# Kernel tuning notes

Measured on AMD Instinct MI355X. Metric: run time of the kernel, lower is better.

The kernel has to match this reference:

```python
import jax, jax.numpy as jnp
import numpy as np

L = 2000          # number of residues (sequence length)
FEATURES_L = 2048 # config.features_L pad target
W = 7             # config.window_size
D = 54            # per-residue feature dim after bert_lin
H = 3             # attention heads
HD = D // H       # head dim = 18
CH = 32           # conv hidden channels
KS = (3, 5, 7)    # config.kernels


def setup_inputs() -> dict:
    key = jax.random.key(0)
    ks = jax.random.split(key, 20)
    n = lambda k, s, sc=0.02: jax.random.normal(k, s, jnp.float32) * sc
    return {
        'beft_f': jax.random.normal(ks[0], (L, 1024), jnp.float32),
        'pssm_f': jax.random.normal(ks[1], (L, 20), jnp.float32),
        'hmm_f': jax.random.normal(ks[2], (L, 30), jnp.float32),
        'dssp_f': jax.random.normal(ks[3], (L, 14), jnp.float32),
        'W_bert': n(ks[4], (1024, D)), 'b_bert': jnp.zeros((D,), jnp.float32),
        'ln_g1': jnp.ones((D,), jnp.float32), 'ln_b1': jnp.zeros((D,), jnp.float32),
        'ln_g2': jnp.ones((D,), jnp.float32), 'ln_b2': jnp.zeros((D,), jnp.float32),
        'conv1_w': n(ks[5], (CH, 1, 3, 1), 0.1), 'conv1_b': n(ks[6], (CH,), 0.1),
        'prelu_a': jnp.array(0.25, jnp.float32),
        'conv2_w': n(ks[7], (CH, 1, 5, 1), 0.1), 'conv2_b': n(ks[8], (CH,), 0.1),
        'conv3_w': n(ks[9], (CH, 1, 7, 1), 0.1), 'conv3_b': n(ks[10], (CH,), 0.1),
        'W1': n(ks[11], (972, 256)), 'b1': jnp.zeros((256,), jnp.float32),
        'W2': n(ks[12], (CH * 256, 256)), 'b2': jnp.zeros((256,), jnp.float32),
    }


def _ln(x, g, b, eps=1e-5):
    m = x.mean(-1, keepdims=True)
    v = ((x - m) ** 2).mean(-1, keepdims=True)
    return (x - m) * jax.lax.rsqrt(v + eps) * g + b


def _attn(x, g, b):
    # x: (L, W, D); no qkv projections, no 1/sqrt(d) scaling (as in source)
    qh = x.reshape(x.shape[0], W, H, HD)
    s = jnp.einsum('bqhd,bkhd->bhqk', qh, qh)
    p = jax.nn.softmax(s, axis=-1)
    o = jnp.einsum('bhqk,bkhd->bqhd', p, qh).reshape(x.shape[0], W, D)
    return _ln(o, g, b)


def _conv_branch(x, w, bias, k, act):
    pad = (k - 1) // 2
    c = jax.lax.conv_general_dilated(x, w, (1, 1), ((pad, pad), (0, 0)),
                                     dimension_numbers=('NCHW', 'OIHW', 'NCHW'))
    c = act(c + bias[None, :, None, None])
    c = jax.lax.reduce_window(c, -jnp.inf, jax.lax.max,
                              (1, 1, k, 1), (1, 1, 1, 1), 'VALID')
    return c.reshape(c.shape[0], CH, -1)  # (FEATURES_L, 32, (W-k+1)*2D)


def _forward(beft_f, W_bert, b_bert, ln_g1, ln_b1, ln_g2, ln_b2,
             conv1_w, conv1_b, prelu_a, conv2_w, conv2_b, conv3_w, conv3_b,
             W1, b1, W2, b2):
    f = beft_f @ W_bert + b_bert  # (L, 54)
    # sliding-window gather replicating the source python loop exactly:
    # interior rows i in (W, L-W): window = f[i-4 : i+3]; boundary rows: [f[i], 0...0]
    i = jnp.arange(L)
    j = jnp.arange(W)
    gidx = jnp.clip(i[:, None] - (W // 2 + 1) + j[None, :], 0, L - 1)
    win_int = f[gidx]                                   # (L, 7, 54)
    win_bnd = jnp.zeros((L, W, D), f.dtype).at[:, 0].set(f)
    boundary = (i <= W) | (i + W >= L)
    new_f = jnp.where(boundary[:, None, None], win_bnd, win_int)
    sf = _attn(new_f, ln_g1, ln_b1)
    sf = _attn(sf, ln_g2, ln_b2)
    cat = jnp.concatenate([new_f, sf], axis=2)          # (L, 7, 108)
    x = jnp.pad(cat, ((0, FEATURES_L - L), (0, 0), (0, 0)))[:, None]  # (FL,1,7,108)
    prelu = lambda z: jnp.where(z >= 0, z, prelu_a * z)
    feats = jnp.concatenate([
        _conv_branch(x, conv1_w, conv1_b, KS[0], prelu),
        _conv_branch(x, conv2_w, conv2_b, KS[1], jax.nn.relu),
        _conv_branch(x, conv3_w, conv3_b, KS[2], jax.nn.relu)], axis=2)  # (FL,32,972)
    y = feats[:L] @ W1 + b1                             # (L, 32, 256)
    y = y.reshape(L, CH * 256) @ W2 + b2                # (L, 256)
    return jnp.where(y >= 0, y, 0.01 * y)               # leaky_relu


def reference(beft_f, pssm_f, hmm_f, dssp_f, W_bert, b_bert, ln_g1, ln_b1,
              ln_g2, ln_b2, conv1_w, conv1_b, prelu_a, conv2_w, conv2_b,
              conv3_w, conv3_b, W1, b1, W2, b2):
    # pssm_f / hmm_f / dssp_f are accepted but unused in the source forward
    return _forward(beft_f, W_bert, b_bert, ln_g1, ln_b1, ln_g2, ln_b2,
                    conv1_w, conv1_b, prelu_a, conv2_w, conv2_b,
                    conv3_w, conv3_b, W1, b1, W2, b2)
```

## Files before the change

### kernel.cpp

```cpp
#include <hip/hip_runtime.h>

#define L_RES 2000
#define DF 54
#define WIN 7

typedef short bf16x8 __attribute__((ext_vector_type(8)));
typedef float f32x4 __attribute__((ext_vector_type(4)));
typedef unsigned short ushort8v __attribute__((ext_vector_type(8)));

__device__ __forceinline__ unsigned short f2bf(float f) {
    unsigned int u = __float_as_uint(f);
    unsigned int r = (u + 0x7FFFu + ((u >> 16) & 1u)) >> 16;
    return (unsigned short)r;
}
__device__ __forceinline__ float bf2f(unsigned short h) {
    return __uint_as_float(((unsigned int)h) << 16);
}

__global__ __launch_bounds__(256) void split_beft(const float* __restrict__ beft,
                                                  unsigned short* __restrict__ A2) {
    int l = blockIdx.x;
    int t = threadIdx.x;
    unsigned short* row = A2 + (size_t)l * 3072;
    for (int k = t; k < 1024; k += 256) {
        unsigned short hi = 0, lo = 0;
        if (l < L_RES) {
            float x = beft[(size_t)l * 1024 + k];
            hi = f2bf(x);
            lo = f2bf(x - bf2f(hi));
        }
        row[k] = hi;
        row[1024 + k] = lo;
        row[2048 + k] = hi;
    }
}

__global__ __launch_bounds__(256) void b2t_build(const float* __restrict__ Wb,
                                                 unsigned short* __restrict__ B2T) {
    int idx = blockIdx.x * 256 + threadIdx.x;
    int n = idx / 3072, col = idx % 3072;
    int seg = col >> 10, k = col & 1023;
    unsigned short r = 0;
    if (n < DF) {
        float v = Wb[(size_t)k * DF + n];
        unsigned short hi = f2bf(v);
        r = (seg < 2) ? hi : f2bf(v - bf2f(hi));
    }
    B2T[idx] = r;
}

__global__ __launch_bounds__(256) void bert_mfma(const unsigned short* __restrict__ A2,
                                                 const unsigned short* __restrict__ B2T,
                                                 const float* __restrict__ bb,
                                                 float* __restrict__ f) {
    __shared__ unsigned short ldsA[128 * 64];
    __shared__ unsigned short ldsB[64 * 64];
    int t = threadIdx.x, w = t >> 6, lane = t & 63;
    int m0 = blockIdx.x * 128;
    int wr = w >> 1, wc = w & 1;
    int arow = lane & 15, kgrp = lane >> 4;

    const unsigned short* aS[4]; const unsigned short* bS[2];
    int aD[4], bD[2];
    #pragma unroll
    for (int j = 0; j < 4; ++j) {
        int s = j * 256 + t, r = s >> 3, c = s & 7;
        aS[j] = A2 + (size_t)(m0 + r) * 3072 + c * 8;
        aD[j] = r * 64 + ((c ^ (r & 7)) * 8);
    }
    #pragma unroll
    for (int j = 0; j < 2; ++j) {
        int s = j * 256 + t, r = s >> 3, c = s & 7;
        bS[j] = B2T + (size_t)r * 3072 + c * 8;
        bD[j] = r * 64 + ((c ^ (r & 7)) * 8);
    }
    f32x4 acc[4][2];
    #pragma unroll
    for (int mi = 0; mi < 4; ++mi)
        #pragma unroll
        for (int ni = 0; ni < 2; ++ni) acc[mi][ni] = (f32x4)(0.f);

    ushort8v va[4], vb[2];
    #pragma unroll
    for (int j = 0; j < 4; ++j) va[j] = *(const ushort8v*)(aS[j]);
    #pragma unroll
    for (int j = 0; j < 2; ++j) vb[j] = *(const ushort8v*)(bS[j]);

    for (int ks = 0; ks < 48; ++ks) {
        __syncthreads();
        #pragma unroll
        for (int j = 0; j < 4; ++j) *(ushort8v*)&ldsA[aD[j]] = va[j];
        #pragma unroll
        for (int j = 0; j < 2; ++j) *(ushort8v*)&ldsB[bD[j]] = vb[j];
        __syncthreads();
        if (ks + 1 < 48) {
            #pragma unroll
            for (int j = 0; j < 4; ++j) va[j] = *(const ushort8v*)(aS[j] + (ks + 1) * 64);
            #pragma unroll
            for (int j = 0; j < 2; ++j) vb[j] = *(const ushort8v*)(bS[j] + (ks + 1) * 64);
        }
        #pragma unroll
        for (int kk = 0; kk < 2; ++kk) {
            int chunk = kk * 4 + kgrp;
            bf16x8 af[4], bfr[2];
            #pragma unroll
            for (int mi = 0; mi < 4; ++mi) {
                int rl = wr * 64 + mi * 16 + arow;
                af[mi] = *(const bf16x8*)&ldsA[rl * 64 + ((chunk ^ (rl & 7)) * 8)];
            }
            #pragma unroll
            for (int ni = 0; ni < 2; ++ni) {
                int rl = wc * 32 + ni * 16 + arow;
                bfr[ni] = *(const bf16x8*)&ldsB[rl * 64 + ((chunk ^ (rl & 7)) * 8)];
            }
            #pragma unroll
            for (int mi = 0; mi < 4; ++mi)
                #pragma unroll
                for (int ni = 0; ni < 2; ++ni)
                    acc[mi][ni] = __builtin_amdgcn_mfma_f32_16x16x32_bf16(af[mi], bfr[ni], acc[mi][ni], 0, 0, 0);
        }
    }
    #pragma unroll
    for (int ni = 0; ni < 2; ++ni) {
        int n = wc * 32 + ni * 16 + arow;
        if (n < DF) {
            float bv = bb[n];
            #pragma unroll
            for (int mi = 0; mi < 4; ++mi)
                #pragma unroll
                for (int r = 0; r < 4; ++r) {
                    int m = m0 + wr * 64 + mi * 16 + kgrp * 4 + r;
                    if (m < L_RES) f[(size_t)m * DF + n] = acc[mi][ni][r] + bv;
                }
        }
    }
}

__device__ __forceinline__ void attn_layer_w(const float (*in)[DF], float (*out)[DF],
                                             float (*s)[WIN][WIN],
                                             const float* __restrict__ g,
                                             const float* __restrict__ b,
                                             float* mm, float* vv, int lane) {
    for (int idx = lane; idx < 3 * WIN * WIN; idx += 64) {
        int h = idx / 49, r = idx % 49, q = r / WIN, k = r % WIN;
        float sum = 0.f;
        #pragma unroll
        for (int d = 0; d < 18; ++d) sum = fmaf(in[q][h * 18 + d], in[k][h * 18 + d], sum);
        s[h][q][k] = sum;
    }
    __syncthreads();
    for (int idx = lane; idx < 3 * WIN; idx += 64) {
        int h = idx / WIN, q = idx % WIN;
        float mx = s[h][q][0];
        #pragma unroll
        for (int k = 1; k < WIN; ++k) mx = fmaxf(mx, s[h][q][k]);
        float e[WIN], sum = 0.f;
        #pragma unroll
        for (int k = 0; k < WIN; ++k) { e[k] = expf(s[h][q][k] - mx); sum += e[k]; }
        float inv = 1.f / sum;
        #pragma unroll
        for (int k = 0; k < WIN; ++k) s[h][q][k] = e[k] * inv;
    }
    __syncthreads();
    for (int idx = lane; idx < WIN * DF; idx += 64) {
        int q = idx / DF, c = idx % DF, h = c / 18;
        float sum = 0.f;
        #pragma unroll
        for (int k = 0; k < WIN; ++k) sum = fmaf(s[h][q][k], in[k][c], sum);
        out[q][c] = sum;
    }
    __syncthreads();
    for (int q = lane; q < WIN; q += 64) {
        float m = 0.f;
        for (int c = 0; c < DF; ++c) m += out[q][c];
        m *= (1.f / DF);
        float v = 0.f;
        for (int c = 0; c < DF; ++c) { float d0 = out[q][c] - m; v = fmaf(d0, d0, v); }
        v *= (1.f / DF);
        mm[q] = m; vv[q] = rsqrtf(v + 1e-5f);
    }
    __syncthreads();
    for (int idx = lane; idx < WIN * DF; idx += 64) {
        int q = idx / DF, c = idx % DF;
        out[q][c] = (out[q][c] - mm[q]) * vv[q] * g[c] + b[c];
    }
    __syncthreads();
}

__global__ __launch_bounds__(256) void window_attn4(const float* __restrict__ f,
                                                    const float* __restrict__ g1,
                                                    const float* __restrict__ b1,
                                                    const float* __restrict__ g2,
                                                    const float* __restrict__ b2,
                                                    float* __restrict__ cat) {
    int wv = threadIdx.x >> 6, lane = threadIdx.x & 63;
    int l = blockIdx.x * 4 + wv;
    __shared__ float w[4][WIN][DF], o1[4][WIN][DF], o2[4][WIN][DF];
    __shared__ float s[4][3][WIN][WIN];
    __shared__ float mm[4][WIN], vvv[4][WIN];
    bool boundary = (l <= WIN) || (l + WIN >= L_RES);
    for (int idx = lane; idx < WIN * DF; idx += 64) {
        int j = idx / DF, d = idx % DF;
        w[wv][j][d] = boundary ? (j == 0 ? f[(size_t)l * DF + d] : 0.f)
                               : f[(size_t)(l - 4 + j) * DF + d];
    }
    __syncthreads();
    attn_layer_w(w[wv], o1[wv], s[wv], g1, b1, mm[wv], vvv[wv], lane);
    attn_layer_w(o1[wv], o2[wv], s[wv], g2, b2, mm[wv], vvv[wv], lane);
    for (int idx = lane; idx < WIN * DF; idx += 64) {
        int j = idx / DF, d = idx % DF;
        cat[(size_t)l * 756 + j * 108 + d] = w[wv][j][d];
        cat[(size_t)l * 756 + j * 108 + DF + d] = o2[wv][j][d];
    }
}

__global__ __launch_bounds__(256) void transpose_to_bf16(const float* __restrict__ src,
                                                         unsigned short* __restrict__ dst,
                                                         int M, int N, int Mpad) {
    __shared__ float tile[32][33];
    int m0 = blockIdx.x * 32, n0 = blockIdx.y * 32;
    int c = threadIdx.x % 32, r0 = threadIdx.x / 32;
    #pragma unroll
    for (int rr = 0; rr < 4; ++rr) {
        int r = r0 + rr * 8, m = m0 + r;
        tile[r][c] = (m < M) ? src[(size_t)m * N + n0 + c] : 0.f;
    }
    __syncthreads();
    #pragma unroll
    for (int rr = 0; rr < 4; ++rr) {
        int r = r0 + rr * 8;
        dst[(size_t)(n0 + r) * Mpad + m0 + c] = f2bf(tile[c][r]);
    }
}

__global__ __launch_bounds__(256) void zero_pad_rows(unsigned int* __restrict__ p) {
    int i = blockIdx.x * 256 + threadIdx.x;
    if (i < 196608) p[i] = 0u;
}

__global__ __launch_bounds__(256) void conv_pool(
        const float* __restrict__ cat,
        const float* __restrict__ c1w, const float* __restrict__ c1b,
        const float* __restrict__ pa_p,
        const float* __restrict__ c2w, const float* __restrict__ c2b,
        const float* __restrict__ c3w, const float* __restrict__ c3b,
        unsigned short* __restrict__ Ap, int lbase) {
    int l = lbase + blockIdx.x;
    int t = threadIdx.x;
    __shared__ float catl[756];
    for (int i = t; i < 756; i += 256) catl[i] = cat[(size_t)l * 756 + i];
    __syncthreads();
    float pa = pa_p[0];
    size_t rowbase = (size_t)blockIdx.x * 32;
    for (int idx = t; idx < 3456; idx += 256) {
        int c = idx / 108, d = idx - c * 108;
        unsigned short* Arow = Ap + (rowbase + c) * 1024;
        float col[WIN];
        #pragma unroll
        for (int h = 0; h < WIN; ++h) col[h] = catl[h * 108 + d];
        {
            float w0 = c1w[c * 3], w1 = c1w[c * 3 + 1], w2 = c1w[c * 3 + 2], bb = c1b[c];
            float v[WIN];
            #pragma unroll
            for (int h = 0; h < WIN; ++h) {
                float sum = bb;
                if (h >= 1) sum = fmaf(w0, col[h - 1], sum);
                sum = fmaf(w1, col[h], sum);
                if (h <= 5) sum = fmaf(w2, col[h + 1], sum);
                v[h] = sum >= 0.f ? sum : pa * sum;
            }
            #pragma unroll
            for (int p = 0; p < 5; ++p)
                Arow[p * 108 + d] = f2bf(fmaxf(fmaxf(v[p], v[p + 1]), v[p + 2]));
        }
        {
            float wg[5], bb = c2b[c];
            #pragma unroll
            for (int x = 0; x < 5; ++x) wg[x] = c2w[c * 5 + x];
            float v[WIN];
            #pragma unroll
            for (int h = 0; h < WIN; ++h) {
                float sum = bb;
                #pragma unroll
                for (int x = 0; x < 5; ++x) {
                    int hh = h + x - 2;
                    if (hh >= 0 && hh <= 6) sum = fmaf(wg[x], col[hh], sum);
                }
                v[h] = fmaxf(sum, 0.f);
            }
            #pragma unroll
            for (int p = 0; p < 3; ++p) {
                float mx = v[p];
                #pragma unroll
                for (int r = 1; r < 5; ++r) mx = fmaxf(mx, v[p + r]);
                Arow[540 + p * 108 + d] = f2bf(mx);
            }
        }
        {
            float wg[7], bb = c3b[c];
            #pragma unroll
            for (int x = 0; x < 7; ++x) wg[x] = c3w[c * 7 + x];
            float mx = 0.f;
            #pragma unroll
            for (int h = 0; h < WIN; ++h) {
                float sum = bb;
                #pragma unroll
                for (int x = 0; x < 7; ++x) {
                    int hh = h + x - 3;
                    if (hh >= 0 && hh <= 6) sum = fmaf(wg[x], col[hh], sum);
                }
                mx = fmaxf(mx, fmaxf(sum, 0.f));
            }
            Arow[864 + d] = f2bf(mx);
        }
    }
    for (int i = t; i < 832; i += 256) {
        int r = i / 26, q = i - r * 26;
        *(unsigned int*)&Ap[(rowbase + r) * 1024 + 972 + q * 2] = 0u;
    }
}

template<bool EPI_BF16, int ZBITS>
__global__ __launch_bounds__(512) void gemm_tile8(
        const unsigned short* __restrict__ A, long lda,
        const unsigned short* __restrict__ B, long ldb,
        int nk, const float* __restrict__ bias,
        unsigned short* __restrict__ outB, float* __restrict__ outF,
        long outRowBase) {
    __shared__ unsigned short ldsA[128 * 64];
    __shared__ unsigned short ldsB[256 * 64];
    int t = threadIdx.x, w = t >> 6, lane = t & 63;
    int bid = blockIdx.x;
    int z = bid & ((1 << ZBITS) - 1);
    long m0 = (long)(bid >> ZBITS) * 128;
    long koff = (long)z * (long)nk * 64;
    A += koff; B += koff;
    int wr = w >> 2, wc = w & 3;
    int arow = lane & 15, kgrp = lane >> 4;

    const unsigned short* aS[2]; const unsigned short* bS[4];
    int aD[2], bD[4];
    #pragma unroll
    for (int j = 0; j < 2; ++j) {
        int s = j * 512 + t, r = s >> 3, c = s & 7;
        aS[j] = A + (size_t)(m0 + r) * lda + c * 8;
        aD[j] = r * 64 + ((c ^ (r & 7)) * 8);
    }
    #pragma unroll
    for (int j = 0; j < 4; ++j) {
        int s = j * 512 + t, r = s >> 3, c = s & 7;
        bS[j] = B + (size_t)r * ldb + c * 8;
        bD[j] = r * 64 + ((c ^ (r & 7)) * 8);
    }
    f32x4 acc[4][4];
    #pragma unroll
    for (int mi = 0; mi < 4; ++mi)
        #pragma unroll
        for (int ni = 0; ni < 4; ++ni) acc[mi][ni] = (f32x4)(0.f);

    ushort8v va[2], vb[4];
    #pragma unroll
    for (int j = 0; j < 2; ++j) va[j] = *(const ushort8v*)(aS[j]);
    #pragma unroll
    for (int j = 0; j < 4; ++j) vb[j] = *(const ushort8v*)(bS[j]);

    for (int ks = 0; ks < nk; ++ks) {
        __syncthreads();
        #pragma unroll
        for (int j = 0; j < 2; ++j) *(ushort8v*)&ldsA[aD[j]] = va[j];
        #pragma unroll
        for (int j = 0; j < 4; ++j) *(ushort8v*)&ldsB[bD[j]] = vb[j];
        __syncthreads();
        if (ks + 1 < nk) {
            #pragma unroll
            for (int j = 0; j < 2; ++j) va[j] = *(const ushort8v*)(aS[j] + (ks + 1) * 64);
            #pragma unroll
            for (int j = 0; j < 4; ++j) vb[j] = *(const ushort8v*)(bS[j] + (ks + 1) * 64);
        }
        #pragma unroll
        for (int kk = 0; kk < 2; ++kk) {
            int chunk = kk * 4 + kgrp;
            bf16x8 af[4], bfr[4];
            #pragma unroll
            for (int mi = 0; mi < 4; ++mi) {
                int rl = wr * 64 + mi * 16 + arow;
                af[mi] = *(const bf16x8*)&ldsA[rl * 64 + ((chunk ^ (rl & 7)) * 8)];
            }
            #pragma unroll
            for (int ni = 0; ni < 4; ++ni) {
                int rl = wc * 64 + ni * 16 + arow;
                bfr[ni] = *(const bf16x8*)&ldsB[rl * 64 + ((chunk ^ (rl & 7)) * 8)];
            }
            #pragma unroll
            for (int mi = 0; mi < 4; ++mi)
                #pragma unroll
                for (int ni = 0; ni < 4; ++ni)
                    acc[mi][ni] = __builtin_amdgcn_mfma_f32_16x16x32_bf16(af[mi], bfr[ni], acc[mi][ni], 0, 0, 0);
        }
    }
    #pragma unroll
    for (int ni = 0; ni < 4; ++ni) {
        int n = wc * 64 + ni * 16 + arow;
        float bv = EPI_BF16 ? bias[n] : 0.f;
        #pragma unroll
        for (int mi = 0; mi < 4; ++mi)
            #pragma unroll
            for (int r = 0; r < 4; ++r) {
                long m = m0 + wr * 64 + mi * 16 + kgrp * 4 + r;
                if (EPI_BF16)
                    outB[(outRowBase + m) * 256 + n] = f2bf(acc[mi][ni][r] + bv);
                else
                    outF[((long)z * 2048 + m) * 256 + n] = acc[mi][ni][r];
            }
    }
}

__global__ __launch_bounds__(256) void reduce2(const float* __restrict__ part,
                                               const float* __restrict__ b2v,
                                               float* __restrict__ out) {
    int l = blockIdx.x, n = threadIdx.x;
    float sum = b2v[n];
    #pragma unroll
    for (int s = 0; s < 8; ++s) sum += part[((size_t)s * 2048 + l) * 256 + n];
    out[(size_t)l * 256 + n] = sum >= 0.f ? sum : 0.01f * sum;
}

extern "C" void kernel_launch(void* const* d_in, const int* in_sizes, int n_in,
                              void* d_out, int out_size, void* d_ws, size_t ws_size,
                              hipStream_t stream) {
    const float* beft = (const float*)d_in[0];
    const float* Wb  = (const float*)d_in[4];
    const float* bb  = (const float*)d_in[5];
    const float* g1  = (const float*)d_in[6];
    const float* b1  = (const float*)d_in[7];
    const float* g2  = (const float*)d_in[8];
    const float* b2  = (const float*)d_in[9];
    const float* c1w = (const float*)d_in[10];
    const float* c1b = (const float*)d_in[11];
    const float* pa  = (const float*)d_in[12];
    const float* c2w = (const float*)d_in[13];
    const float* c2b = (const float*)d_in[14];
    const float* c3w = (const float*)d_in[15];
    const float* c3b = (const float*)d_in[16];
    const float* W1  = (const float*)d_in[17];
    const float* b1v = (const float*)d_in[18];
    const float* W2  = (const float*)d_in[19];
    const float* b2v = (const float*)d_in[20];
    float* out = (float*)d_out;
    char* ws = (char*)d_ws;

    float*          f    = (float*)(ws + 0);
    float*          cat  = (float*)(ws + 524288);
    unsigned short* W1T  = (unsigned short*)(ws + 8388608);
    unsigned short* W2T  = (unsigned short*)(ws + 8912896);
    unsigned short* y1   = (unsigned short*)(ws + 13107200);
    unsigned short* A2   = (unsigned short*)(ws + 13107200);
    unsigned short* B2T  = (unsigned short*)(ws + 25690112);
    unsigned short* Ap   = (unsigned short*)(ws + 46661632);
    float*          part = (float*)(ws + 46661632);

    long avail = (long)ws_size - 46661632L;
    long tpc = avail / (128L * 1024L * 2L);
    if (tpc < 1) tpc = 1;
    if (tpc > 500) tpc = 500;

    split_beft<<<2048, 256, 0, stream>>>(beft, A2);
    b2t_build<<<768, 256, 0, stream>>>(Wb, B2T);
    bert_mfma<<<16, 256, 0, stream>>>(A2, B2T, bb, f);
    window_attn4<<<500, 256, 0, stream>>>(f, g1, b1, g2, b2, cat);
    transpose_to_bf16<<<dim3(32, 8), 256, 0, stream>>>(W1, W1T, 972, 256, 1024);
    transpose_to_bf16<<<dim3(256, 8), 256, 0, stream>>>(W2, W2T, 8192, 256, 8192);
    zero_pad_rows<<<768, 256, 0, stream>>>((unsigned int*)(y1 + (size_t)2000 * 8192));

    for (long t0 = 0; t0 < 500; t0 += tpc) {
        long nt = (500 - t0 < tpc) ? (500 - t0) : tpc;
        conv_pool<<<(int)(nt * 4), 256, 0, stream>>>(cat, c1w, c1b, pa, c2w, c2b,
                                                     c3w, c3b, Ap, (int)(t0 * 4));
        gemm_tile8<true, 0><<<(int)nt, 512, 0, stream>>>(
            Ap, 1024, W1T, 1024, 16, b1v, y1, nullptr, t0 * 128);
    }
    gemm_tile8<false, 3><<<128, 512, 0, stream>>>(
        y1, 8192, W2T, 8192, 16, nullptr, nullptr, part, 0);
    reduce2<<<L_RES, 256, 0, stream>>>(part, b2v, out);
}
```

Measured before the change: 180.6 us.

## Split-K the bert GEMM, stage conv output in LDS, use direct global-to-LDS loads

```diff
diff --git a/kernel.cpp b/kernel.cpp
--- a/kernel.cpp
+++ b/kernel.cpp
@@ -15,6 +15,11 @@
 }
 __device__ __forceinline__ float bf2f(unsigned short h) {
     return __uint_as_float(((unsigned int)h) << 16);
+}
+__device__ __forceinline__ void gload16(const unsigned short* g, unsigned short* l) {
+    __builtin_amdgcn_global_load_lds(
+        (const __attribute__((address_space(1))) void*)g,
+        (__attribute__((address_space(3))) void*)l, 16, 0, 0);
 }
 
 __global__ __launch_bounds__(256) void split_beft(const float* __restrict__ beft,
@@ -51,12 +56,13 @@
 
 __global__ __launch_bounds__(256) void bert_mfma(const unsigned short* __restrict__ A2,
                                                  const unsigned short* __restrict__ B2T,
-                                                 const float* __restrict__ bb,
-                                                 float* __restrict__ f) {
+                                                 float* __restrict__ bpart) {
     __shared__ unsigned short ldsA[128 * 64];
     __shared__ unsigned short ldsB[64 * 64];
     int t = threadIdx.x, w = t >> 6, lane = t & 63;
     int m0 = blockIdx.x * 128;
+    int z = blockIdx.y;
+    long koff = (long)z * 768;
     int wr = w >> 1, wc = w & 1;
     int arow = lane & 15, kgrp = lane >> 4;
 
@@ -65,13 +71,13 @@
     #pragma unroll
     for (int j = 0; j < 4; ++j) {
         int s = j * 256 + t, r = s >> 3, c = s & 7;
-        aS[j] = A2 + (size_t)(m0 + r) * 3072 + c * 8;
+        aS[j] = A2 + koff + (size_t)(m0 + r) * 3072 + c * 8;
         aD[j] = r * 64 + ((c ^ (r & 7)) * 8);
     }
     #pragma unroll
     for (int j = 0; j < 2; ++j) {
         int s = j * 256 + t, r = s >> 3, c = s & 7;
-        bS[j] = B2T + (size_t)r * 3072 + c * 8;
+        bS[j] = B2T + koff + (size_t)r * 3072 + c * 8;
         bD[j] = r * 64 + ((c ^ (r & 7)) * 8);
     }
     f32x4 acc[4][2];
@@ -86,14 +92,14 @@
     #pragma unroll
     for (int j = 0; j < 2; ++j) vb[j] = *(const ushort8v*)(bS[j]);
 
-    for (int ks = 0; ks < 48; ++ks) {
+    for (int ks = 0; ks < 12; ++ks) {
         __syncthreads();
         #pragma unroll
         for (int j = 0; j < 4; ++j) *(ushort8v*)&ldsA[aD[j]] = va[j];
         #pragma unroll
         for (int j = 0; j < 2; ++j) *(ushort8v*)&ldsB[bD[j]] = vb[j];
         __syncthreads();
-        if (ks + 1 < 48) {
+        if (ks + 1 < 12) {
             #pragma unroll
             for (int j = 0; j < 4; ++j) va[j] = *(const ushort8v*)(aS[j] + (ks + 1) * 64);
             #pragma unroll
@@ -123,16 +129,25 @@
     #pragma unroll
     for (int ni = 0; ni < 2; ++ni) {
         int n = wc * 32 + ni * 16 + arow;
-        if (n < DF) {
-            float bv = bb[n];
-            #pragma unroll
-            for (int mi = 0; mi < 4; ++mi)
-                #pragma unroll
-                for (int r = 0; r < 4; ++r) {
-                    int m = m0 + wr * 64 + mi * 16 + kgrp * 4 + r;
-                    if (m < L_RES) f[(size_t)m * DF + n] = acc[mi][ni][r] + bv;
-                }
-        }
+        #pragma unroll
+        for (int mi = 0; mi < 4; ++mi)
+            #pragma unroll
+            for (int r = 0; r < 4; ++r) {
+                int m = m0 + wr * 64 + mi * 16 + kgrp * 4 + r;
+                bpart[((size_t)z * 2048 + m) * 64 + n] = acc[mi][ni][r];
+            }
+    }
+}
+
+__global__ __launch_bounds__(64) void bert_reduce(const float* __restrict__ bpart,
+                                                  const float* __restrict__ bb,
+                                                  float* __restrict__ f) {
+    int l = blockIdx.x, n = threadIdx.x;
+    if (n < DF) {
+        float s = bb[n];
+        #pragma unroll
+        for (int z = 0; z < 4; ++z) s += bpart[((size_t)z * 2048 + l) * 64 + n];
+        f[(size_t)l * DF + n] = s;
     }
 }
 
@@ -248,13 +263,17 @@
     int l = lbase + blockIdx.x;
     int t = threadIdx.x;
     __shared__ float catl[756];
+    __shared__ unsigned short Al[32 * 1024];
     for (int i = t; i < 756; i += 256) catl[i] = cat[(size_t)l * 756 + i];
+    for (int i = t; i < 832; i += 256) {
+        int r = i / 26, q = i - r * 26;
+        *(unsigned int*)&Al[r * 1024 + 972 + q * 2] = 0u;
+    }
     __syncthreads();
     float pa = pa_p[0];
-    size_t rowbase = (size_t)blockIdx.x * 32;
     for (int idx = t; idx < 3456; idx += 256) {
         int c = idx / 108, d = idx - c * 108;
-        unsigned short* Arow = Ap + (rowbase + c) * 1024;
+        unsigned short* Arow = Al + c * 1024;
         float col[WIN];
         #pragma unroll
         for (int h = 0; h < WIN; ++h) col[h] = catl[h * 108 + d];
@@ -314,9 +333,12 @@
             Arow[864 + d] = f2bf(mx);
         }
     }
-    for (int i = t; i < 832; i += 256) {
-        int r = i / 26, q = i - r * 26;
-        *(unsigned int*)&Ap[(rowbase + r) * 1024 + 972 + q * 2] = 0u;
+    __syncthreads();
+    unsigned short* dst = Ap + (size_t)blockIdx.x * 32768;
+    #pragma unroll
+    for (int i = 0; i < 16; ++i) {
+        int e = (i * 256 + t) * 8;
+        *(ushort8v*)&dst[e] = *(const ushort8v*)&Al[e];
     }
 }
 
@@ -337,20 +359,22 @@
     A += koff; B += koff;
     int wr = w >> 2, wc = w & 3;
     int arow = lane & 15, kgrp = lane >> 4;
-
-    const unsigned short* aS[2]; const unsigned short* bS[4];
-    int aD[2], bD[4];
+    int ra = lane >> 3, cc = lane & 7;
+    int csw = (cc ^ ra) * 8;
+
+    const unsigned short* gA[2]; const unsigned short* gB[4];
+    unsigned short* dA[2]; unsigned short* dB[4];
     #pragma unroll
     for (int j = 0; j < 2; ++j) {
-        int s = j * 512 + t, r = s >> 3, c = s & 7;
-        aS[j] = A + (size_t)(m0 + r) * lda + c * 8;
-        aD[j] = r * 64 + ((c ^ (r & 7)) * 8);
+        int rbase = j * 64 + w * 8;
+        gA[j] = A + (size_t)(m0 + rbase + ra) * lda + csw;
+        dA[j] = &ldsA[rbase * 64];
     }
     #pragma unroll
     for (int j = 0; j < 4; ++j) {
-        int s = j * 512 + t, r = s >> 3, c = s & 7;
-        bS[j] = B + (size_t)r * ldb + c * 8;
-        bD[j] = r * 64 + ((c ^ (r & 7)) * 8);
+        int rbase = j * 64 + w * 8;
+        gB[j] = B + (size_t)(rbase + ra) * ldb + csw;
+        dB[j] = &ldsB[rbase * 64];
     }
     f32x4 acc[4][4];
     #pragma unroll
@@ -358,25 +382,12 @@
         #pragma unroll
         for (int ni = 0; ni < 4; ++ni) acc[mi][ni] = (f32x4)(0.f);
 
-    ushort8v va[2], vb[4];
-    #pragma unroll
-    for (int j = 0; j < 2; ++j) va[j] = *(const ushort8v*)(aS[j]);
-    #pragma unroll
-    for (int j = 0; j < 4; ++j) vb[j] = *(const ushort8v*)(bS[j]);
-
     for (int ks = 0; ks < nk; ++ks) {
+        #pragma unroll
+        for (int j = 0; j < 2; ++j) gload16(gA[j] + ks * 64, dA[j]);
+        #pragma unroll
+        for (int j = 0; j < 4; ++j) gload16(gB[j] + ks * 64, dB[j]);
         __syncthreads();
-        #pragma unroll
-        for (int j = 0; j < 2; ++j) *(ushort8v*)&ldsA[aD[j]] = va[j];
-        #pragma unroll
-        for (int j = 0; j < 4; ++j) *(ushort8v*)&ldsB[bD[j]] = vb[j];
-        __syncthreads();
-        if (ks + 1 < nk) {
-            #pragma unroll
-            for (int j = 0; j < 2; ++j) va[j] = *(const ushort8v*)(aS[j] + (ks + 1) * 64);
-            #pragma unroll
-            for (int j = 0; j < 4; ++j) vb[j] = *(const ushort8v*)(bS[j] + (ks + 1) * 64);
-        }
         #pragma unroll
         for (int kk = 0; kk < 2; ++kk) {
             int chunk = kk * 4 + kgrp;
@@ -397,6 +408,7 @@
                 for (int ni = 0; ni < 4; ++ni)
                     acc[mi][ni] = __builtin_amdgcn_mfma_f32_16x16x32_bf16(af[mi], bfr[ni], acc[mi][ni], 0, 0, 0);
         }
+        __syncthreads();
     }
     #pragma unroll
     for (int ni = 0; ni < 4; ++ni) {
@@ -456,6 +468,7 @@
     unsigned short* y1   = (unsigned short*)(ws + 13107200);
     unsigned short* A2   = (unsigned short*)(ws + 13107200);
     unsigned short* B2T  = (unsigned short*)(ws + 25690112);
+    float*          bpart= (float*)(ws + 46661632);
     unsigned short* Ap   = (unsigned short*)(ws + 46661632);
     float*          part = (float*)(ws + 46661632);
 
@@ -466,7 +479,8 @@
 
     split_beft<<<2048, 256, 0, stream>>>(beft, A2);
     b2t_build<<<768, 256, 0, stream>>>(Wb, B2T);
-    bert_mfma<<<16, 256, 0, stream>>>(A2, B2T, bb, f);
+    bert_mfma<<<dim3(16, 4), 256, 0, stream>>>(A2, B2T, bpart);
+    bert_reduce<<<L_RES, 64, 0, stream>>>(bpart, bb, f);
     window_attn4<<<500, 256, 0, stream>>>(f, g1, b1, g2, b2, cat);
     transpose_to_bf16<<<dim3(32, 8), 256, 0, stream>>>(W1, W1T, 972, 256, 1024);
     transpose_to_bf16<<<dim3(256, 8), 256, 0, stream>>>(W2, W2T, 8192, 256, 8192);
```

New measurement: 169.4 us. 6.2% less time.
